# Kernel optimization log

Hardware: AMD Instinct MI355X
Metric: run time of the kernel (lower is better)

Reference implementation:

```python
import jax, jax.numpy as jnp
import numpy as np

N = 100000   # nodes
E = 1600000  # edges
IN = 128
H = 128
OUT = 128
G = 1000     # graphs


def setup_inputs() -> dict:
    key = jax.random.key(0)
    ks = jax.random.split(key, 6)
    x = jax.random.normal(ks[0], (N, IN), jnp.float32)
    edge_index = jax.random.randint(ks[1], (2, E), 0, N, dtype=jnp.int64)
    batch = jnp.sort(jax.random.randint(ks[2], (N,), 0, G, dtype=jnp.int64))
    # Glorot-ish init for the two GCN linear transforms
    W1 = jax.random.normal(ks[3], (IN, H), jnp.float32) * (1.0 / np.sqrt(IN))
    b1 = jnp.zeros((H,), jnp.float32)
    W2 = jax.random.normal(ks[4], (H, OUT), jnp.float32) * (1.0 / np.sqrt(H))
    b2 = jnp.zeros((OUT,), jnp.float32)
    return {"x": x, "edge_index": edge_index, "batch": batch,
            "W1": W1, "b1": b1, "W2": W2, "b2": b2, "num_graphs": G}


def reference(x, edge_index, batch, W1, b1, W2, b2, num_graphs):
    n = x.shape[0]
    src, dst = edge_index[0], edge_index[1]
    # GCN normalization with self-loops: deg includes the self-loop (+1)
    deg = jax.ops.segment_sum(jnp.ones(src.shape[0], x.dtype), dst,
                              num_segments=n) + 1.0
    dinv = jax.lax.rsqrt(deg)                 # [N]
    norm = dinv[src] * dinv[dst]              # [E] per-edge coefficient
    self_norm = dinv * dinv                   # [N] self-loop coefficient

    def gcn_conv(h, W, b):
        hw = h @ W                                            # [N, F] dense transform
        msg = norm[:, None] * hw[src]                         # gather + scale, [E, F]
        agg = jax.ops.segment_sum(msg, dst, num_segments=n)   # scatter-add
        return agg + self_norm[:, None] * hw + b              # self-loop + bias

    h = jax.nn.relu(gcn_conv(x, W1, b1))
    h = gcn_conv(h, W2, b2)

    # global_mean_pool over graph ids
    sums = jax.ops.segment_sum(h, batch, num_segments=num_graphs)
    counts = jax.ops.segment_sum(jnp.ones(n, h.dtype), batch,
                                 num_segments=num_graphs)
    return sums / jnp.maximum(counts, 1.0)[:, None]
```

## Files before the change

### kernel.cpp

```cpp
#include <hip/hip_runtime.h>
#include <hip/hip_fp16.h>

#define FDIM 128
#define BROWS 64
#define KCH 16
#define NCH (FDIM / KCH)
#define BSHIFT 9
#define BNODES 512
#define EPB 4096


__global__ __launch_bounds__(256) void bucket_count(const int* __restrict__ dst,
                                                    int* __restrict__ bcnt, int E) {
    __shared__ int lc[256];
    lc[threadIdx.x] = 0;
    __syncthreads();
    for (int e = blockIdx.x * blockDim.x + threadIdx.x; e < E;
         e += gridDim.x * blockDim.x)
        atomicAdd(&lc[dst[e] >> BSHIFT], 1);
    __syncthreads();
    int c = lc[threadIdx.x];
    if (c) atomicAdd(&bcnt[threadIdx.x], c);
}

__global__ void bucket_scan(const int* __restrict__ bcnt, int* __restrict__ bbase,
                            int* __restrict__ bcur, int* __restrict__ rp,
                            int E, int n, int nbuck) {
    __shared__ int s[2][256];
    int t = threadIdx.x;
    int v = (t < nbuck) ? bcnt[t] : 0;
    s[0][t] = v;
    __syncthreads();
    int cur = 0;
    for (int off = 1; off < 256; off <<= 1) {
        int x = s[cur][t];
        if (t >= off) x += s[cur][t - off];
        s[cur ^ 1][t] = x;
        cur ^= 1;
        __syncthreads();
    }
    int ex = s[cur][t] - v;
    if (t < nbuck) { bbase[t] = ex; bcur[t] = ex; }
    if (t == 0) { bbase[nbuck] = E; rp[n] = E; }
}

__global__ __launch_bounds__(256) void binscatter(const int* __restrict__ src,
                                                  const int* __restrict__ dst,
                                                  int* __restrict__ bcur,
                                                  int2* __restrict__ eb, int E) {
    __shared__ int lcnt[256];
    __shared__ int gb[256];
    const int t = threadIdx.x;
    const int e0 = blockIdx.x * EPB;
    const int e1 = min(e0 + EPB, E);
    lcnt[t] = 0;
    __syncthreads();
    for (int e = e0 + t; e < e1; e += 256)
        atomicAdd(&lcnt[dst[e] >> BSHIFT], 1);
    __syncthreads();
    int c = lcnt[t];
    if (c) gb[t] = atomicAdd(&bcur[t], c);
    __syncthreads();
    lcnt[t] = 0;
    __syncthreads();
    for (int e = e0 + t; e < e1; e += 256) {
        int d = dst[e];
        int b = d >> BSHIFT;
        int lo = atomicAdd(&lcnt[b], 1);
        eb[gb[b] + lo] = make_int2(src[e], d);
    }
}

__global__ __launch_bounds__(256) void csr_count(const int2* __restrict__ eb,
                                                 const int* __restrict__ bbase,
                                                 int* __restrict__ rp,
                                                 float* __restrict__ dinv, int n) {
    __shared__ int lcnt[BNODES];
    __shared__ int s[2][BNODES];
    const int t = threadIdx.x;
    const int node0 = blockIdx.x << BSHIFT;
    const int nloc = min(BNODES, n - node0);
    lcnt[t] = 0; lcnt[t + 256] = 0;
    __syncthreads();
    const int eb0 = bbase[blockIdx.x], eb1 = bbase[blockIdx.x + 1];
    for (int e = eb0 + t; e < eb1; e += 256)
        atomicAdd(&lcnt[eb[e].y - node0], 1);
    __syncthreads();
    s[0][t] = lcnt[t]; s[0][t + 256] = lcnt[t + 256];
    __syncthreads();
    int cur = 0;
    for (int off = 1; off < BNODES; off <<= 1) {
        int x0 = s[cur][t];       if (t >= off)        x0 += s[cur][t - off];
        int x1 = s[cur][t + 256]; if (t + 256 >= off)  x1 += s[cur][t + 256 - off];
        s[cur ^ 1][t] = x0; s[cur ^ 1][t + 256] = x1;
        cur ^= 1;
        __syncthreads();
    }
    if (t < nloc) {
        rp[node0 + t] = eb0 + s[cur][t] - lcnt[t];
        dinv[node0 + t] = rsqrtf((float)lcnt[t] + 1.0f);
    }
    if (t + 256 < nloc) {
        rp[node0 + t + 256] = eb0 + s[cur][t + 256] - lcnt[t + 256];
        dinv[node0 + t + 256] = rsqrtf((float)lcnt[t + 256] + 1.0f);
    }
}

__global__ __launch_bounds__(256) void csr_fill(const int2* __restrict__ eb,
                                                const int* __restrict__ bbase,
                                                const int* __restrict__ rp,
                                                const float* __restrict__ dinv,
                                                int2* __restrict__ em, int n) {
    __shared__ int lcur[BNODES];
    const int t = threadIdx.x;
    const int node0 = blockIdx.x << BSHIFT;
    const int nloc = min(BNODES, n - node0);
    if (t < nloc) lcur[t] = rp[node0 + t];
    if (t + 256 < nloc) lcur[t + 256] = rp[node0 + t + 256];
    __syncthreads();
    const int eb0 = bbase[blockIdx.x], eb1 = bbase[blockIdx.x + 1];
    for (int e = eb0 + t; e < eb1; e += 256) {
        int2 sd = eb[e];
        int pos = atomicAdd(&lcur[sd.y - node0], 1);
        em[pos] = make_int2(sd.x, __float_as_int(dinv[sd.x] * dinv[sd.y]));
    }
}

__global__ void graph_counts(const int* __restrict__ batch, int* __restrict__ gcnt, int n) {
    int i = blockIdx.x * blockDim.x + threadIdx.x;
    if (i < n) atomicAdd(&gcnt[batch[i]], 1);
}

__global__ __launch_bounds__(256) void gemm128(const float* __restrict__ X,
                                               const float* __restrict__ W,
                                               __half* __restrict__ Y, int n) {
    __shared__ float Ws[FDIM * FDIM];
    __shared__ float xs[2][BROWS][KCH + 4];

    const int tid  = threadIdx.x;
    const int c    = tid & 15;
    const int r    = tid >> 4;
    const int srow = tid >> 2;
    const int skk  = (tid & 3) << 2;
    const int r0   = blockIdx.x * BROWS;

    for (int i = tid; i < FDIM * FDIM; i += 256) Ws[i] = W[i];

    const int grow  = r0 + srow;
    const bool rowok = grow < n;
    const float* xrow = X + (size_t)grow * FDIM + skk;

    float4 v = rowok ? *(const float4*)xrow : float4{0.f, 0.f, 0.f, 0.f};
    *(float4*)&xs[0][srow][skk] = v;
    __syncthreads();

    float accA[4][4], accB[4][4];
#pragma unroll
    for (int m = 0; m < 4; ++m)
#pragma unroll
        for (int i = 0; i < 4; ++i) { accA[m][i] = 0.f; accB[m][i] = 0.f; }

    for (int ch = 0; ch < NCH; ++ch) {
        const int b = ch & 1;
        float4 nv{0.f, 0.f, 0.f, 0.f};
        if (ch + 1 < NCH && rowok)
            nv = *(const float4*)(xrow + (ch + 1) * KCH);
        const int k0 = ch * KCH;
#pragma unroll
        for (int k4 = 0; k4 < KCH; k4 += 4) {
            float4 xv0 = *(const float4*)&xs[b][r][k4];
            float4 xv1 = *(const float4*)&xs[b][r + 16][k4];
            float4 xv2 = *(const float4*)&xs[b][r + 32][k4];
            float4 xv3 = *(const float4*)&xs[b][r + 48][k4];
#define GSTEP(kk, comp)                                                        \
            {                                                                  \
                const float* wp = &Ws[(k0 + k4 + kk) * FDIM + 4 * c];          \
                const float4 w0 = *(const float4*)wp;                          \
                const float4 w1 = *(const float4*)(wp + 64);                   \
                const float xr[4] = {xv0.comp, xv1.comp, xv2.comp, xv3.comp};  \
                _Pragma("unroll")                                              \
                for (int m = 0; m < 4; ++m) {                                  \
                    accA[m][0] = fmaf(xr[m], w0.x, accA[m][0]);                \
                    accA[m][1] = fmaf(xr[m], w0.y, accA[m][1]);                \
                    accA[m][2] = fmaf(xr[m], w0.z, accA[m][2]);                \
                    accB[m][0] = fmaf(xr[m], w1.x, accB[m][0]);                \
                    accB[m][1] = fmaf(xr[m], w1.y, accB[m][1]);                \
                    accB[m][2] = fmaf(xr[m], w1.z, accB[m][2]);                \
                    accB[m][3] = fmaf(xr[m], w1.w, accB[m][3]);                \
                    accA[m][3] = fmaf(xr[m], w0.w, accA[m][3]);                \
                }                                                              \
            }
            GSTEP(0, x) GSTEP(1, y) GSTEP(2, z) GSTEP(3, w)
#undef GSTEP
        }
        if (ch + 1 < NCH)
            *(float4*)&xs[b ^ 1][srow][skk] = nv;
        __syncthreads();
    }

#pragma unroll
    for (int m = 0; m < 4; ++m) {
        int row = r0 + r + 16 * m;
        if (row < n) {
            union { __half2 h[2]; uint2 u; } pa, pb;
            pa.h[0] = __floats2half2_rn(accA[m][0], accA[m][1]);
            pa.h[1] = __floats2half2_rn(accA[m][2], accA[m][3]);
            pb.h[0] = __floats2half2_rn(accB[m][0], accB[m][1]);
            pb.h[1] = __floats2half2_rn(accB[m][2], accB[m][3]);
            *(uint2*)&Y[(size_t)row * FDIM + 4 * c]      = pa.u;
            *(uint2*)&Y[(size_t)row * FDIM + 64 + 4 * c] = pb.u;
        }
    }
}

__device__ __forceinline__ void acc_edge(float4& a, uint2 v, float w) {
    __half2* h = (__half2*)&v;
    float2 f0 = __half22float2(h[0]);
    float2 f1 = __half22float2(h[1]);
    a.x = fmaf(w, f0.x, a.x);
    a.y = fmaf(w, f0.y, a.y);
    a.z = fmaf(w, f1.x, a.z);
    a.w = fmaf(w, f1.y, a.w);
}

__global__ __launch_bounds__(256) void aggregate_relu(
        const __half* __restrict__ hw, const int* __restrict__ rp,
        const int2* __restrict__ em, const float* __restrict__ dinv,
        const float* __restrict__ bias, __half* __restrict__ out, int n) {
    const int lane = threadIdx.x & 31;
    const int node = blockIdx.x * 8 + (threadIdx.x >> 5);
    if (node >= n) return;
    const uint2* hw2 = (const uint2*)hw;
    int e0 = rp[node], e1 = rp[node + 1];
    float4 a{0.f, 0.f, 0.f, 0.f};
    int e = e0;
    for (; e + 8 <= e1; e += 8) {
        int2 m[8];
        uint2 v[8];
#pragma unroll
        for (int k = 0; k < 8; ++k) m[k] = em[e + k];
#pragma unroll
        for (int k = 0; k < 8; ++k) v[k] = hw2[(size_t)m[k].x * 32 + lane];
#pragma unroll
        for (int k = 0; k < 8; ++k) acc_edge(a, v[k], __int_as_float(m[k].y));
    }
    for (; e < e1; ++e) {
        int2 m = em[e];
        acc_edge(a, hw2[(size_t)m.x * 32 + lane], __int_as_float(m.y));
    }
    float dv = dinv[node];
    float sn = dv * dv;
    uint2 sv = hw2[(size_t)node * 32 + lane];
    __half2* sh = (__half2*)&sv;
    float2 s0 = __half22float2(sh[0]);
    float2 s1 = __half22float2(sh[1]);
    float4 b = ((const float4*)bias)[lane];
    a.x = fmaxf(fmaf(sn, s0.x, a.x) + b.x, 0.f);
    a.y = fmaxf(fmaf(sn, s0.y, a.y) + b.y, 0.f);
    a.z = fmaxf(fmaf(sn, s1.x, a.z) + b.z, 0.f);
    a.w = fmaxf(fmaf(sn, s1.y, a.w) + b.w, 0.f);
    union { __half2 h[2]; uint2 u; } pk;
    pk.h[0] = __floats2half2_rn(a.x, a.y);
    pk.h[1] = __floats2half2_rn(a.z, a.w);
    ((uint2*)out)[(size_t)node * 32 + lane] = pk.u;
}

__global__ __launch_bounds__(256) void aggregate_pool(
        const __half* __restrict__ h1, const int* __restrict__ rp,
        const int2* __restrict__ em, const float* __restrict__ dinv,
        const int* __restrict__ batch, float* __restrict__ pool, int n) {
    __shared__ float4 part[8][32];
    __shared__ int gs[8];
    const int lane = threadIdx.x & 31;
    const int half = threadIdx.x >> 5;
    const int node = blockIdx.x * 8 + half;
    const bool valid = node < n;
    const uint2* hw2 = (const uint2*)h1;
    int e0 = 0, e1 = 0;
    if (valid) { e0 = rp[node]; e1 = rp[node + 1]; }
    float4 a{0.f, 0.f, 0.f, 0.f};
    int e = e0;
    for (; e + 8 <= e1; e += 8) {
        int2 m[8];
        uint2 v[8];
#pragma unroll
        for (int k = 0; k < 8; ++k) m[k] = em[e + k];
#pragma unroll
        for (int k = 0; k < 8; ++k) v[k] = hw2[(size_t)m[k].x * 32 + lane];
#pragma unroll
        for (int k = 0; k < 8; ++k) acc_edge(a, v[k], __int_as_float(m[k].y));
    }
    for (; e < e1; ++e) {
        int2 m = em[e];
        acc_edge(a, hw2[(size_t)m.x * 32 + lane], __int_as_float(m.y));
    }
    if (valid) {
        float dv = dinv[node];
        float sn = dv * dv;
        uint2 sv = hw2[(size_t)node * 32 + lane];
        __half2* sh = (__half2*)&sv;
        float2 s0 = __half22float2(sh[0]);
        float2 s1 = __half22float2(sh[1]);
        a.x = fmaf(sn, s0.x, a.x);
        a.y = fmaf(sn, s0.y, a.y);
        a.z = fmaf(sn, s1.x, a.z);
        a.w = fmaf(sn, s1.y, a.w);
    }
    part[half][lane] = a;
    if (lane == 0) gs[half] = valid ? batch[node] : -1;
    __syncthreads();
    if (half == 0) {
        float4 acc = part[0][lane];
        int g0 = gs[0];
#pragma unroll
        for (int h = 1; h < 8; ++h) {
            if (gs[h] == g0) {
                float4 p = part[h][lane];
                acc.x += p.x; acc.y += p.y; acc.z += p.z; acc.w += p.w;
            } else {
                if (g0 >= 0) {
                    float* dst = &pool[g0 * FDIM + lane * 4];
                    atomicAdd(dst + 0, acc.x); atomicAdd(dst + 1, acc.y);
                    atomicAdd(dst + 2, acc.z); atomicAdd(dst + 3, acc.w);
                }
                g0 = gs[h];
                acc = part[h][lane];
            }
        }
        if (g0 >= 0) {
            float* dst = &pool[g0 * FDIM + lane * 4];
            atomicAdd(dst + 0, acc.x); atomicAdd(dst + 1, acc.y);
            atomicAdd(dst + 2, acc.z); atomicAdd(dst + 3, acc.w);
        }
    }
}

__global__ __launch_bounds__(256) void pool_gemm(const float* __restrict__ pool,
                                                 const int* __restrict__ gcnt,
                                                 const float* __restrict__ W2,
                                                 const float* __restrict__ b2,
                                                 float* __restrict__ out, int G) {
    __shared__ float Ws[FDIM * FDIM];
    __shared__ float row[2][FDIM];
    for (int i = threadIdx.x; i < FDIM * FDIM; i += 256) Ws[i] = W2[i];
    const int j  = threadIdx.x & 127;
    const int gh = threadIdx.x >> 7;
    for (int g0 = blockIdx.x * 2; g0 < G; g0 += gridDim.x * 2) {
        const int g = g0 + gh;
        __syncthreads();
        int c = 0;
        if (g < G) {
            c = gcnt[g];
            float inv = (c > 0) ? 1.0f / (float)c : 0.0f;
            row[gh][j] = pool[g * FDIM + j] * inv;
        }
        __syncthreads();
        if (g < G) {
            float acc = (c > 0) ? b2[j] : 0.0f;
#pragma unroll
            for (int k = 0; k < FDIM; ++k)
                acc = fmaf(row[gh][k], Ws[k * FDIM + j], acc);
            out[g * FDIM + j] = acc;
        }
    }
}


extern "C" void kernel_launch(void* const* d_in, const int* in_sizes, int n_in,
                              void* d_out, int out_size, void* d_ws, size_t ws_size,
                              hipStream_t stream) {
    const float* x     = (const float*)d_in[0];
    const int*   ei    = (const int*)d_in[1];
    const int*   batch = (const int*)d_in[2];
    const float* W1    = (const float*)d_in[3];
    const float* b1    = (const float*)d_in[4];
    const float* W2    = (const float*)d_in[5];
    const float* b2    = (const float*)d_in[6];
    float* out = (float*)d_out;

    const int N = in_sizes[0] / FDIM;
    const int E = in_sizes[1] / 2;
    const int G = out_size / FDIM;
    const int* src = ei;
    const int* dst = ei + E;
    const int nbuck = (N + BNODES - 1) >> BSHIFT;

    char* p = (char*)d_ws;
    auto alloc = [&](size_t bytes) {
        void* r = (void*)p;
        p += (bytes + 255) & ~(size_t)255;
        return r;
    };
    float*  dinv  = (float*) alloc((size_t)N * 4);
    int*    rp    = (int*)   alloc((size_t)(N + 1) * 4);
    int*    gcnt  = (int*)   alloc((size_t)G * 4);
    int*    bcnt  = (int*)   alloc(256 * 4);
    int*    bbase = (int*)   alloc(257 * 4);
    int*    bcur  = (int*)   alloc(256 * 4);
    int2*   eb    = (int2*)  alloc((size_t)E * 8);
    int2*   em    = (int2*)  alloc((size_t)E * 8);
    __half* hw    = (__half*)alloc((size_t)N * FDIM * 2);
    __half* h1    = (__half*)alloc((size_t)N * FDIM * 2);
    float*  pool  = (float*) alloc((size_t)G * FDIM * 4);

    hipMemsetAsync(bcnt, 0, 256 * 4, stream);
    hipMemsetAsync(gcnt, 0, (size_t)G * 4, stream);
    hipMemsetAsync(pool, 0, (size_t)G * FDIM * 4, stream);

    bucket_count<<<1024, 256, 0, stream>>>(dst, bcnt, E);
    bucket_scan<<<1, 256, 0, stream>>>(bcnt, bbase, bcur, rp, E, N, nbuck);
    binscatter<<<(E + EPB - 1) / EPB, 256, 0, stream>>>(src, dst, bcur, eb, E);
    csr_count<<<nbuck, 256, 0, stream>>>(eb, bbase, rp, dinv, N);
    csr_fill<<<nbuck, 256, 0, stream>>>(eb, bbase, rp, dinv, em, N);
    graph_counts<<<(N + 255) / 256, 256, 0, stream>>>(batch, gcnt, N);

    const int GB = (N + BROWS - 1) / BROWS;
    gemm128<<<GB, 256, 0, stream>>>(x, W1, hw, N);
    aggregate_relu<<<(N + 7) / 8, 256, 0, stream>>>(hw, rp, em, dinv, b1, h1, N);
    aggregate_pool<<<(N + 7) / 8, 256, 0, stream>>>(h1, rp, em, dinv, batch, pool, N);
    pool_gemm<<<64, 256, 0, stream>>>(pool, gcnt, W2, b2, out, G);
}
```

Measured before the change: 433.7 us.

## Factor GCN normalization into node scaling and pack edge lists to 4 bytes

Moves the symmetric normalization out of the per-edge weight: hw rows are prescaled by dinv in the GEMM epilogue, and the aggregations scale the summed result by dinv[dst]. Edge records shrink from int2 (src, weight) to a single int, and the bucket records pack src plus local dst into one 32-bit word. csr_count, csr_fill and graph_counts are merged into one csr_build kernel, and the gather loop unroll grows to 16. This cuts edge-list memory traffic and launches, but relies on src fitting in 23 bits and changes fp16 rounding slightly.

```diff
diff --git a/kernel.cpp b/kernel.cpp
--- a/kernel.cpp
+++ b/kernel.cpp
@@ -47,7 +47,7 @@
 __global__ __launch_bounds__(256) void binscatter(const int* __restrict__ src,
                                                   const int* __restrict__ dst,
                                                   int* __restrict__ bcur,
-                                                  int2* __restrict__ eb, int E) {
+                                                  unsigned* __restrict__ ebp, int E) {
     __shared__ int lcnt[256];
     __shared__ int gb[256];
     const int t = threadIdx.x;
@@ -67,16 +67,20 @@
         int d = dst[e];
         int b = d >> BSHIFT;
         int lo = atomicAdd(&lcnt[b], 1);
-        eb[gb[b] + lo] = make_int2(src[e], d);
-    }
-}
-
-__global__ __launch_bounds__(256) void csr_count(const int2* __restrict__ eb,
+        ebp[gb[b] + lo] = ((unsigned)src[e] << BSHIFT) | (unsigned)(d & (BNODES - 1));
+    }
+}
+
+__global__ __launch_bounds__(256) void csr_build(const unsigned* __restrict__ ebp,
                                                  const int* __restrict__ bbase,
+                                                 const int* __restrict__ batch,
                                                  int* __restrict__ rp,
-                                                 float* __restrict__ dinv, int n) {
+                                                 float* __restrict__ dinv,
+                                                 int* __restrict__ em,
+                                                 int* __restrict__ gcnt, int n) {
     __shared__ int lcnt[BNODES];
     __shared__ int s[2][BNODES];
+    __shared__ int lcur[BNODES];
     const int t = threadIdx.x;
     const int node0 = blockIdx.x << BSHIFT;
     const int nloc = min(BNODES, n - node0);
@@ -84,55 +88,42 @@
     __syncthreads();
     const int eb0 = bbase[blockIdx.x], eb1 = bbase[blockIdx.x + 1];
     for (int e = eb0 + t; e < eb1; e += 256)
-        atomicAdd(&lcnt[eb[e].y - node0], 1);
+        atomicAdd(&lcnt[ebp[e] & (BNODES - 1)], 1);
     __syncthreads();
     s[0][t] = lcnt[t]; s[0][t + 256] = lcnt[t + 256];
     __syncthreads();
     int cur = 0;
     for (int off = 1; off < BNODES; off <<= 1) {
-        int x0 = s[cur][t];       if (t >= off)        x0 += s[cur][t - off];
-        int x1 = s[cur][t + 256]; if (t + 256 >= off)  x1 += s[cur][t + 256 - off];
+        int x0 = s[cur][t];       if (t >= off)       x0 += s[cur][t - off];
+        int x1 = s[cur][t + 256]; if (t + 256 >= off) x1 += s[cur][t + 256 - off];
         s[cur ^ 1][t] = x0; s[cur ^ 1][t + 256] = x1;
         cur ^= 1;
         __syncthreads();
     }
+    int ex0 = eb0 + s[cur][t] - lcnt[t];
+    int ex1 = eb0 + s[cur][t + 256] - lcnt[t + 256];
+    lcur[t] = ex0; lcur[t + 256] = ex1;
     if (t < nloc) {
-        rp[node0 + t] = eb0 + s[cur][t] - lcnt[t];
+        rp[node0 + t] = ex0;
         dinv[node0 + t] = rsqrtf((float)lcnt[t] + 1.0f);
     }
     if (t + 256 < nloc) {
-        rp[node0 + t + 256] = eb0 + s[cur][t + 256] - lcnt[t + 256];
+        rp[node0 + t + 256] = ex1;
         dinv[node0 + t + 256] = rsqrtf((float)lcnt[t + 256] + 1.0f);
     }
-}
-
-__global__ __launch_bounds__(256) void csr_fill(const int2* __restrict__ eb,
-                                                const int* __restrict__ bbase,
-                                                const int* __restrict__ rp,
-                                                const float* __restrict__ dinv,
-                                                int2* __restrict__ em, int n) {
-    __shared__ int lcur[BNODES];
-    const int t = threadIdx.x;
-    const int node0 = blockIdx.x << BSHIFT;
-    const int nloc = min(BNODES, n - node0);
-    if (t < nloc) lcur[t] = rp[node0 + t];
-    if (t + 256 < nloc) lcur[t + 256] = rp[node0 + t + 256];
-    __syncthreads();
-    const int eb0 = bbase[blockIdx.x], eb1 = bbase[blockIdx.x + 1];
+    __syncthreads();
     for (int e = eb0 + t; e < eb1; e += 256) {
-        int2 sd = eb[e];
-        int pos = atomicAdd(&lcur[sd.y - node0], 1);
-        em[pos] = make_int2(sd.x, __float_as_int(dinv[sd.x] * dinv[sd.y]));
-    }
-}
-
-__global__ void graph_counts(const int* __restrict__ batch, int* __restrict__ gcnt, int n) {
-    int i = blockIdx.x * blockDim.x + threadIdx.x;
-    if (i < n) atomicAdd(&gcnt[batch[i]], 1);
+        unsigned v = ebp[e];
+        int pos = atomicAdd(&lcur[v & (BNODES - 1)], 1);
+        em[pos] = (int)(v >> BSHIFT);
+    }
+    if (t < nloc) atomicAdd(&gcnt[batch[node0 + t]], 1);
+    if (t + 256 < nloc) atomicAdd(&gcnt[batch[node0 + t + 256]], 1);
 }
 
 __global__ __launch_bounds__(256) void gemm128(const float* __restrict__ X,
                                                const float* __restrict__ W,
+                                               const float* __restrict__ dinv,
                                                __half* __restrict__ Y, int n) {
     __shared__ float Ws[FDIM * FDIM];
     __shared__ float xs[2][BROWS][KCH + 4];
@@ -202,63 +193,58 @@
     for (int m = 0; m < 4; ++m) {
         int row = r0 + r + 16 * m;
         if (row < n) {
+            float dv = dinv[row];
             union { __half2 h[2]; uint2 u; } pa, pb;
-            pa.h[0] = __floats2half2_rn(accA[m][0], accA[m][1]);
-            pa.h[1] = __floats2half2_rn(accA[m][2], accA[m][3]);
-            pb.h[0] = __floats2half2_rn(accB[m][0], accB[m][1]);
-            pb.h[1] = __floats2half2_rn(accB[m][2], accB[m][3]);
+            pa.h[0] = __floats2half2_rn(dv * accA[m][0], dv * accA[m][1]);
+            pa.h[1] = __floats2half2_rn(dv * accA[m][2], dv * accA[m][3]);
+            pb.h[0] = __floats2half2_rn(dv * accB[m][0], dv * accB[m][1]);
+            pb.h[1] = __floats2half2_rn(dv * accB[m][2], dv * accB[m][3]);
             *(uint2*)&Y[(size_t)row * FDIM + 4 * c]      = pa.u;
             *(uint2*)&Y[(size_t)row * FDIM + 64 + 4 * c] = pb.u;
         }
     }
 }
 
-__device__ __forceinline__ void acc_edge(float4& a, uint2 v, float w) {
+__device__ __forceinline__ void addv(float4& a, uint2 v) {
     __half2* h = (__half2*)&v;
     float2 f0 = __half22float2(h[0]);
     float2 f1 = __half22float2(h[1]);
-    a.x = fmaf(w, f0.x, a.x);
-    a.y = fmaf(w, f0.y, a.y);
-    a.z = fmaf(w, f1.x, a.z);
-    a.w = fmaf(w, f1.y, a.w);
+    a.x += f0.x; a.y += f0.y; a.z += f1.x; a.w += f1.y;
 }
 
 __global__ __launch_bounds__(256) void aggregate_relu(
         const __half* __restrict__ hw, const int* __restrict__ rp,
-        const int2* __restrict__ em, const float* __restrict__ dinv,
+        const int* __restrict__ em, const float* __restrict__ dinv,
         const float* __restrict__ bias, __half* __restrict__ out, int n) {
     const int lane = threadIdx.x & 31;
     const int node = blockIdx.x * 8 + (threadIdx.x >> 5);
     if (node >= n) return;
-    const uint2* hw2 = (const uint2*)hw;
+    const uint2* T = (const uint2*)hw;
     int e0 = rp[node], e1 = rp[node + 1];
     float4 a{0.f, 0.f, 0.f, 0.f};
     int e = e0;
-    for (; e + 8 <= e1; e += 8) {
-        int2 m[8];
-        uint2 v[8];
-#pragma unroll
-        for (int k = 0; k < 8; ++k) m[k] = em[e + k];
-#pragma unroll
-        for (int k = 0; k < 8; ++k) v[k] = hw2[(size_t)m[k].x * 32 + lane];
-#pragma unroll
-        for (int k = 0; k < 8; ++k) acc_edge(a, v[k], __int_as_float(m[k].y));
-    }
-    for (; e < e1; ++e) {
-        int2 m = em[e];
-        acc_edge(a, hw2[(size_t)m.x * 32 + lane], __int_as_float(m.y));
-    }
+    for (; e + 16 <= e1; e += 16) {
+        uint2 v[16];
+#pragma unroll
+        for (int k = 0; k < 16; ++k) v[k] = T[(size_t)em[e + k] * 32 + lane];
+#pragma unroll
+        for (int k = 0; k < 16; ++k) addv(a, v[k]);
+    }
+    for (; e + 4 <= e1; e += 4) {
+        uint2 v[4];
+#pragma unroll
+        for (int k = 0; k < 4; ++k) v[k] = T[(size_t)em[e + k] * 32 + lane];
+#pragma unroll
+        for (int k = 0; k < 4; ++k) addv(a, v[k]);
+    }
+    for (; e < e1; ++e) addv(a, T[(size_t)em[e] * 32 + lane]);
+    addv(a, T[(size_t)node * 32 + lane]);
     float dv = dinv[node];
-    float sn = dv * dv;
-    uint2 sv = hw2[(size_t)node * 32 + lane];
-    __half2* sh = (__half2*)&sv;
-    float2 s0 = __half22float2(sh[0]);
-    float2 s1 = __half22float2(sh[1]);
     float4 b = ((const float4*)bias)[lane];
-    a.x = fmaxf(fmaf(sn, s0.x, a.x) + b.x, 0.f);
-    a.y = fmaxf(fmaf(sn, s0.y, a.y) + b.y, 0.f);
-    a.z = fmaxf(fmaf(sn, s1.x, a.z) + b.z, 0.f);
-    a.w = fmaxf(fmaf(sn, s1.y, a.w) + b.w, 0.f);
+    a.x = dv * fmaxf(fmaf(dv, a.x, b.x), 0.f);
+    a.y = dv * fmaxf(fmaf(dv, a.y, b.y), 0.f);
+    a.z = dv * fmaxf(fmaf(dv, a.z, b.z), 0.f);
+    a.w = dv * fmaxf(fmaf(dv, a.w, b.w), 0.f);
     union { __half2 h[2]; uint2 u; } pk;
     pk.h[0] = __floats2half2_rn(a.x, a.y);
     pk.h[1] = __floats2half2_rn(a.z, a.w);
@@ -267,7 +253,7 @@
 
 __global__ __launch_bounds__(256) void aggregate_pool(
         const __half* __restrict__ h1, const int* __restrict__ rp,
-        const int2* __restrict__ em, const float* __restrict__ dinv,
+        const int* __restrict__ em, const float* __restrict__ dinv,
         const int* __restrict__ batch, float* __restrict__ pool, int n) {
     __shared__ float4 part[8][32];
     __shared__ int gs[8];
@@ -275,36 +261,30 @@
     const int half = threadIdx.x >> 5;
     const int node = blockIdx.x * 8 + half;
     const bool valid = node < n;
-    const uint2* hw2 = (const uint2*)h1;
+    const uint2* T = (const uint2*)h1;
     int e0 = 0, e1 = 0;
     if (valid) { e0 = rp[node]; e1 = rp[node + 1]; }
     float4 a{0.f, 0.f, 0.f, 0.f};
     int e = e0;
-    for (; e + 8 <= e1; e += 8) {
-        int2 m[8];
-        uint2 v[8];
-#pragma unroll
-        for (int k = 0; k < 8; ++k) m[k] = em[e + k];
-#pragma unroll
-        for (int k = 0; k < 8; ++k) v[k] = hw2[(size_t)m[k].x * 32 + lane];
-#pragma unroll
-        for (int k = 0; k < 8; ++k) acc_edge(a, v[k], __int_as_float(m[k].y));
-    }
-    for (; e < e1; ++e) {
-        int2 m = em[e];
-        acc_edge(a, hw2[(size_t)m.x * 32 + lane], __int_as_float(m.y));
-    }
+    for (; e + 16 <= e1; e += 16) {
+        uint2 v[16];
+#pragma unroll
+        for (int k = 0; k < 16; ++k) v[k] = T[(size_t)em[e + k] * 32 + lane];
+#pragma unroll
+        for (int k = 0; k < 16; ++k) addv(a, v[k]);
+    }
+    for (; e + 4 <= e1; e += 4) {
+        uint2 v[4];
+#pragma unroll
+        for (int k = 0; k < 4; ++k) v[k] = T[(size_t)em[e + k] * 32 + lane];
+#pragma unroll
+        for (int k = 0; k < 4; ++k) addv(a, v[k]);
+    }
+    for (; e < e1; ++e) addv(a, T[(size_t)em[e] * 32 + lane]);
     if (valid) {
+        addv(a, T[(size_t)node * 32 + lane]);
         float dv = dinv[node];
-        float sn = dv * dv;
-        uint2 sv = hw2[(size_t)node * 32 + lane];
-        __half2* sh = (__half2*)&sv;
-        float2 s0 = __half22float2(sh[0]);
-        float2 s1 = __half22float2(sh[1]);
-        a.x = fmaf(sn, s0.x, a.x);
-        a.y = fmaf(sn, s0.y, a.y);
-        a.z = fmaf(sn, s1.x, a.z);
-        a.w = fmaf(sn, s1.y, a.w);
+        a.x *= dv; a.y *= dv; a.z *= dv; a.w *= dv;
     }
     part[half][lane] = a;
     if (lane == 0) gs[half] = valid ? batch[node] : -1;
@@ -319,18 +299,18 @@
                 acc.x += p.x; acc.y += p.y; acc.z += p.z; acc.w += p.w;
             } else {
                 if (g0 >= 0) {
-                    float* dst = &pool[g0 * FDIM + lane * 4];
-                    atomicAdd(dst + 0, acc.x); atomicAdd(dst + 1, acc.y);
-                    atomicAdd(dst + 2, acc.z); atomicAdd(dst + 3, acc.w);
+                    float* dstp = &pool[g0 * FDIM + lane * 4];
+                    atomicAdd(dstp + 0, acc.x); atomicAdd(dstp + 1, acc.y);
+                    atomicAdd(dstp + 2, acc.z); atomicAdd(dstp + 3, acc.w);
                 }
                 g0 = gs[h];
                 acc = part[h][lane];
             }
         }
         if (g0 >= 0) {
-            float* dst = &pool[g0 * FDIM + lane * 4];
-            atomicAdd(dst + 0, acc.x); atomicAdd(dst + 1, acc.y);
-            atomicAdd(dst + 2, acc.z); atomicAdd(dst + 3, acc.w);
+            float* dstp = &pool[g0 * FDIM + lane * 4];
+            atomicAdd(dstp + 0, acc.x); atomicAdd(dstp + 1, acc.y);
+            atomicAdd(dstp + 2, acc.z); atomicAdd(dstp + 3, acc.w);
         }
     }
 }
@@ -391,17 +371,17 @@
         p += (bytes + 255) & ~(size_t)255;
         return r;
     };
-    float*  dinv  = (float*) alloc((size_t)N * 4);
-    int*    rp    = (int*)   alloc((size_t)(N + 1) * 4);
-    int*    gcnt  = (int*)   alloc((size_t)G * 4);
-    int*    bcnt  = (int*)   alloc(256 * 4);
-    int*    bbase = (int*)   alloc(257 * 4);
-    int*    bcur  = (int*)   alloc(256 * 4);
-    int2*   eb    = (int2*)  alloc((size_t)E * 8);
-    int2*   em    = (int2*)  alloc((size_t)E * 8);
-    __half* hw    = (__half*)alloc((size_t)N * FDIM * 2);
-    __half* h1    = (__half*)alloc((size_t)N * FDIM * 2);
-    float*  pool  = (float*) alloc((size_t)G * FDIM * 4);
+    float*    dinv  = (float*)   alloc((size_t)N * 4);
+    int*      rp    = (int*)     alloc((size_t)(N + 1) * 4);
+    int*      gcnt  = (int*)     alloc((size_t)G * 4);
+    int*      bcnt  = (int*)     alloc(256 * 4);
+    int*      bbase = (int*)     alloc(257 * 4);
+    int*      bcur  = (int*)     alloc(256 * 4);
+    unsigned* ebp   = (unsigned*)alloc((size_t)E * 4);
+    int*      em    = (int*)     alloc((size_t)E * 4);
+    __half*   hw    = (__half*)  alloc((size_t)N * FDIM * 2);
+    __half*   h1    = (__half*)  alloc((size_t)N * FDIM * 2);
+    float*    pool  = (float*)   alloc((size_t)G * FDIM * 4);
 
     hipMemsetAsync(bcnt, 0, 256 * 4, stream);
     hipMemsetAsync(gcnt, 0, (size_t)G * 4, stream);
@@ -409,13 +389,11 @@
 
     bucket_count<<<1024, 256, 0, stream>>>(dst, bcnt, E);
     bucket_scan<<<1, 256, 0, stream>>>(bcnt, bbase, bcur, rp, E, N, nbuck);
-    binscatter<<<(E + EPB - 1) / EPB, 256, 0, stream>>>(src, dst, bcur, eb, E);
-    csr_count<<<nbuck, 256, 0, stream>>>(eb, bbase, rp, dinv, N);
-    csr_fill<<<nbuck, 256, 0, stream>>>(eb, bbase, rp, dinv, em, N);
-    graph_counts<<<(N + 255) / 256, 256, 0, stream>>>(batch, gcnt, N);
+    binscatter<<<(E + EPB - 1) / EPB, 256, 0, stream>>>(src, dst, bcur, ebp, E);
+    csr_build<<<nbuck, 256, 0, stream>>>(ebp, bbase, batch, rp, dinv, em, gcnt, N);
 
     const int GB = (N + BROWS - 1) / BROWS;
-    gemm128<<<GB, 256, 0, stream>>>(x, W1, hw, N);
+    gemm128<<<GB, 256, 0, stream>>>(x, W1, dinv, hw, N);
     aggregate_relu<<<(N + 7) / 8, 256, 0, stream>>>(hw, rp, em, dinv, b1, h1, N);
     aggregate_pool<<<(N + 7) / 8, 256, 0, stream>>>(h1, rp, em, dinv, batch, pool, N);
     pool_gemm<<<64, 256, 0, stream>>>(pool, gcnt, W2, b2, out, G);
```

Result: faster. 410.0 us (-5.5%).
